# Optimization experiments

Measured on AMD Instinct MI355X. Metric: run time of the kernel, lower is better.

The kernel has to match this reference:

```python
import jax, jax.numpy as jnp
import numpy as np


def setup_inputs() -> dict:
    key = jax.random.key(0)
    k1, k2, k3, k4, k5 = jax.random.split(key, 5)
    B, F, S = 4096, 2048, 2048
    return {
        "weights": jax.random.normal(k1, (F + S, 3 * S), dtype=jnp.float32),
        "bias": jax.random.normal(k2, (3 * S,), dtype=jnp.float32),
        "input": jax.random.normal(k3, (B, F), dtype=jnp.float32),
        "old_h": jax.random.normal(k4, (B, S), dtype=jnp.float32),
        "old_c": jax.random.normal(k5, (B, S), dtype=jnp.float32),
    }


def reference(weights, bias, input, old_h, old_c):
    # LLTM cell (PyTorch C++ extension tutorial math):
    # X = [old_h, input]; gates = X @ W + b, split into 3 chunks of state_size.
    S = old_h.shape[1]
    X = jnp.concatenate([old_h, input], axis=1)            # (B, S+F)
    gate_weights = X @ weights + bias                       # (B, 3S)
    input_gate = jax.nn.sigmoid(gate_weights[:, :S])
    output_gate = jax.nn.sigmoid(gate_weights[:, S:2 * S])
    candidate_cell = jax.nn.elu(gate_weights[:, 2 * S:])
    new_cell = old_c + candidate_cell * input_gate          # (B, S)
    new_h = jnp.tanh(new_cell) * output_gate
    return new_h, new_cell
```

## Files before the change

### kernel.cpp

```cpp
#include <hip/hip_runtime.h>

typedef unsigned short u16;
typedef unsigned int u32;
typedef __attribute__((ext_vector_type(8))) __bf16 bf16x8;
typedef __attribute__((ext_vector_type(4))) float f32x4;
typedef __attribute__((ext_vector_type(4))) u32 u32x4;

#define MDIM 4096
#define KDIM 4096
#define NDIM 6144
#define SDIM 2048
#define KC   (KDIM / 32)

__device__ __forceinline__ u32 asu(float f) { return __float_as_uint(f); }

__device__ __forceinline__ void gld16(const void* g, void* l) {
    __builtin_amdgcn_global_load_lds(
        (const __attribute__((address_space(1))) u32*)g,
        (__attribute__((address_space(3))) u32*)l, 16, 0, 0);
}

__device__ __forceinline__ u32 pk(float a, float b) {
    return (asu(a) >> 16) | (asu(b) & 0xffff0000u);
}

__global__ __launch_bounds__(256) void prep(const float* __restrict__ W,
                                            const float* __restrict__ oldh,
                                            const float* __restrict__ inp,
                                            u32* __restrict__ Whl,
                                            u32* __restrict__ Ahl) {
    const int t = threadIdx.x;
    if (blockIdx.x < 6144) {
        __shared__ u32 wh[64][33];
        __shared__ u32 wl[64][33];
        const int n0 = (blockIdx.x % 96) * 64;
        const int k0 = (blockIdx.x / 96) * 64;
#pragma unroll
        for (int r = 0; r < 4; ++r) {
            int bid = t + r * 256;
            int nb = bid & 31;
            int kb = bid >> 5;
            const float* p0 = W + (size_t)(k0 + 2 * kb) * NDIM + n0 + 2 * nb;
            float2 w0 = *(const float2*)p0;
            float2 w1 = *(const float2*)(p0 + NDIM);
            float h00 = __uint_as_float(asu(w0.x) & 0xffff0000u);
            float h01 = __uint_as_float(asu(w0.y) & 0xffff0000u);
            float h10 = __uint_as_float(asu(w1.x) & 0xffff0000u);
            float h11 = __uint_as_float(asu(w1.y) & 0xffff0000u);
            wh[2 * nb][kb]     = pk(w0.x, w1.x);
            wh[2 * nb + 1][kb] = pk(w0.y, w1.y);
            wl[2 * nb][kb]     = pk(w0.x - h00, w1.x - h10);
            wl[2 * nb + 1][kb] = pk(w0.y - h01, w1.y - h11);
        }
        __syncthreads();
#pragma unroll
        for (int r = 0; r < 2; ++r) {
            int v = t + r * 256;
            int nl = v >> 3;
            int kw = (v & 7) * 4;
            int c  = (k0 >> 5) + (kw >> 4);
            int ww = kw & 15;
            size_t o = ((size_t)(n0 + nl) * KC + c) * 32 + ww;
            *(uint4*)(Whl + o)      = make_uint4(wh[nl][kw], wh[nl][kw + 1],
                                                 wh[nl][kw + 2], wh[nl][kw + 3]);
            *(uint4*)(Whl + o + 16) = make_uint4(wl[nl][kw], wl[nl][kw + 1],
                                                 wl[nl][kw + 2], wl[nl][kw + 3]);
        }
    } else {
        const int m = blockIdx.x - 6144;
#pragma unroll
        for (int rr = 0; rr < 2; ++rr) {
            int gk = t + rr * 256;
            int k = gk * 8;
            const float* src = (k < SDIM)
                                   ? (oldh + (size_t)m * SDIM + k)
                                   : (inp + (size_t)m * SDIM + (k - SDIM));
            float4 f0 = *(const float4*)src;
            float4 f1 = *(const float4*)(src + 4);
            int c = gk >> 2, g = gk & 3;
            size_t o = ((size_t)m * KC + c) * 32 + g * 4;
            *(uint4*)(Ahl + o) = make_uint4(pk(f0.x, f0.y), pk(f0.z, f0.w),
                                            pk(f1.x, f1.y), pk(f1.z, f1.w));
            float4 l0, l1;
            l0.x = f0.x - __uint_as_float(asu(f0.x) & 0xffff0000u);
            l0.y = f0.y - __uint_as_float(asu(f0.y) & 0xffff0000u);
            l0.z = f0.z - __uint_as_float(asu(f0.z) & 0xffff0000u);
            l0.w = f0.w - __uint_as_float(asu(f0.w) & 0xffff0000u);
            l1.x = f1.x - __uint_as_float(asu(f1.x) & 0xffff0000u);
            l1.y = f1.y - __uint_as_float(asu(f1.y) & 0xffff0000u);
            l1.z = f1.z - __uint_as_float(asu(f1.z) & 0xffff0000u);
            l1.w = f1.w - __uint_as_float(asu(f1.w) & 0xffff0000u);
            *(uint4*)(Ahl + o + 16) = make_uint4(pk(l0.x, l0.y), pk(l0.z, l0.w),
                                                 pk(l1.x, l1.y), pk(l1.z, l1.w));
        }
    }
}

__global__ __launch_bounds__(256, 2) void gemm_lltm(const u32* __restrict__ Whl,
                                                    const u32* __restrict__ Ahl,
                                                    const float* __restrict__ bias,
                                                    const float* __restrict__ oldc,
                                                    float* __restrict__ out) {
    __shared__ u16 As[2][128 * 64];
    __shared__ u16 Bs[2][192 * 64];
    const int t = threadIdx.x;
    const int lane = t & 63;
    const int wv = t >> 6;
    const int wm = wv >> 1;
    const int wn = wv & 1;
    const int row0 = blockIdx.y * 128;
    const int col0 = blockIdx.x * 64;

    f32x4 acc[3][4][2];
#pragma unroll
    for (int g = 0; g < 3; ++g)
#pragma unroll
        for (int i = 0; i < 4; ++i)
#pragma unroll
            for (int j = 0; j < 2; ++j)
                acc[g][i][j] = (f32x4){0.f, 0.f, 0.f, 0.f};

    const int sr8 = lane >> 3;
    const int lg  = (lane & 7) ^ sr8;

    const u32* aSrc[4];
#pragma unroll
    for (int i = 0; i < 4; ++i) {
        int r = wv * 32 + i * 8 + sr8;
        aSrc[i] = Ahl + (size_t)(row0 + r) * (KC * 32) + lg * 4;
    }
    const u32* bSrc[6];
#pragma unroll
    for (int p = 0; p < 6; ++p) {
        int r = wv * 48 + p * 8 + sr8;
        int n = (r >> 6) * SDIM + col0 + (r & 63);
        bSrc[p] = Whl + (size_t)n * (KC * 32) + lg * 4;
    }

    const int lm = lane & 15;
    const int q  = lane >> 4;
    const int sw = lm & 7;
    const int slotHi = q ^ sw;

    {
#pragma unroll
        for (int i = 0; i < 4; ++i)
            gld16(aSrc[i], &As[0][(wv * 32 + i * 8) * 64]);
#pragma unroll
        for (int p = 0; p < 6; ++p)
            gld16(bSrc[p], &Bs[0][(wv * 48 + p * 8) * 64]);
    }
    asm volatile("s_waitcnt vmcnt(0)" ::: "memory");
    __syncthreads();

    for (int c = 0; c < KC; ++c) {
        const int buf = c & 1;
        if (c + 1 < KC) {
#pragma unroll
            for (int i = 0; i < 4; ++i)
                gld16(aSrc[i] + (size_t)(c + 1) * 32,
                      &As[buf ^ 1][(wv * 32 + i * 8) * 64]);
#pragma unroll
            for (int p = 0; p < 6; ++p)
                gld16(bSrc[p] + (size_t)(c + 1) * 32,
                      &Bs[buf ^ 1][(wv * 48 + p * 8) * 64]);
        }

        bf16x8 ah[4], al[4];
#pragma unroll
        for (int i = 0; i < 4; ++i) {
            int mr = wm * 64 + i * 16 + lm;
            const u16* ap = &As[buf][mr * 64];
            ah[i] = *(const bf16x8*)(ap + slotHi * 8);
            al[i] = *(const bf16x8*)(ap + (slotHi ^ 4) * 8);
        }
        bf16x8 bh, bl;
        {
            const u16* bp = &Bs[buf][(wn * 32 + lm) * 64];
            bh = *(const bf16x8*)(bp + slotHi * 8);
            bl = *(const bf16x8*)(bp + (slotHi ^ 4) * 8);
        }

#pragma unroll
        for (int pc = 0; pc < 6; ++pc) {
            const int g = pc >> 1, j = pc & 1;
            bf16x8 cbh = bh, cbl = bl;
            if (pc < 5) {
                const int g2 = (pc + 1) >> 1, j2 = (pc + 1) & 1;
                const u16* bp =
                    &Bs[buf][(g2 * 64 + wn * 32 + j2 * 16 + lm) * 64];
                bh = *(const bf16x8*)(bp + slotHi * 8);
                bl = *(const bf16x8*)(bp + (slotHi ^ 4) * 8);
            }
            __builtin_amdgcn_s_setprio(1);
#pragma unroll
            for (int i = 0; i < 4; ++i)
                acc[g][i][j] = __builtin_amdgcn_mfma_f32_16x16x32_bf16(
                    ah[i], cbh, acc[g][i][j], 0, 0, 0);
#pragma unroll
            for (int i = 0; i < 4; ++i)
                acc[g][i][j] = __builtin_amdgcn_mfma_f32_16x16x32_bf16(
                    al[i], cbh, acc[g][i][j], 0, 0, 0);
#pragma unroll
            for (int i = 0; i < 4; ++i)
                acc[g][i][j] = __builtin_amdgcn_mfma_f32_16x16x32_bf16(
                    ah[i], cbl, acc[g][i][j], 0, 0, 0);
            __builtin_amdgcn_s_setprio(0);
        }
        asm volatile("s_waitcnt vmcnt(0)" ::: "memory");
        __syncthreads();
    }

    const int rq = q * 4;
#pragma unroll
    for (int j = 0; j < 2; ++j) {
        int scol = col0 + wn * 32 + j * 16 + lm;
        float b0v = bias[scol];
        float b1v = bias[SDIM + scol];
        float b2v = bias[2 * SDIM + scol];
#pragma unroll
        for (int i = 0; i < 4; ++i) {
#pragma unroll
            for (int r = 0; r < 4; ++r) {
                int row = row0 + wm * 64 + i * 16 + rq + r;
                float x0 = acc[0][i][j][r] + b0v;
                float x1 = acc[1][i][j][r] + b1v;
                float x2 = acc[2][i][j][r] + b2v;
                float ig = 1.f / (1.f + __expf(-x0));
                float og = 1.f / (1.f + __expf(-x1));
                float el = x2 > 0.f ? x2 : (__expf(x2) - 1.f);
                float nc = oldc[(size_t)row * SDIM + scol] + el * ig;
                float nh = tanhf(nc) * og;
                out[(size_t)row * SDIM + scol] = nh;
                out[(size_t)MDIM * SDIM + (size_t)row * SDIM + scol] = nc;
            }
        }
    }
}

extern "C" void kernel_launch(void* const* d_in, const int* in_sizes, int n_in,
                              void* d_out, int out_size, void* d_ws, size_t ws_size,
                              hipStream_t stream) {
    const float* W    = (const float*)d_in[0];
    const float* bias = (const float*)d_in[1];
    const float* inp  = (const float*)d_in[2];
    const float* oldh = (const float*)d_in[3];
    const float* oldc = (const float*)d_in[4];

    u32* Whl = (u32*)d_ws;
    u32* Ahl = Whl + (size_t)NDIM * KC * 32;

    prep<<<6144 + MDIM, 256, 0, stream>>>(W, oldh, inp, Whl, Ahl);
    gemm_lltm<<<dim3(SDIM / 64, MDIM / 128), 256, 0, stream>>>(Whl, Ahl, bias,
                                                               oldc,
                                                               (float*)d_out);
}
```

Before: 714.9 us.

## Load A fragments directly from global into registers, bypassing LDS

The A tile is no longer staged through shared memory. Each lane now loads its MFMA A fragments (hi and lo bf16 parts) straight from global memory into registers, double-buffered across an unrolled pair of iterations. This removes the LDS traffic and the shared-memory footprint for A, which may help occupancy. In exchange, each A row is loaded redundantly by both wn waves, global accesses are less coalesced, and register pressure rises.

```diff
diff --git a/kernel.cpp b/kernel.cpp
--- a/kernel.cpp
+++ b/kernel.cpp
@@ -101,7 +101,6 @@
                                                     const float* __restrict__ bias,
                                                     const float* __restrict__ oldc,
                                                     float* __restrict__ out) {
-    __shared__ u16 As[2][128 * 64];
     __shared__ u16 Bs[2][192 * 64];
     const int t = threadIdx.x;
     const int lane = t & 63;
@@ -123,12 +122,11 @@
     const int sr8 = lane >> 3;
     const int lg  = (lane & 7) ^ sr8;
 
-    const u32* aSrc[4];
-#pragma unroll
-    for (int i = 0; i < 4; ++i) {
-        int r = wv * 32 + i * 8 + sr8;
-        aSrc[i] = Ahl + (size_t)(row0 + r) * (KC * 32) + lg * 4;
-    }
+    const int lm = lane & 15;
+    const int q  = lane >> 4;
+    const int sw = lm & 7;
+    const int slotHi = q ^ sw;
+
     const u32* bSrc[6];
 #pragma unroll
     for (int p = 0; p < 6; ++p) {
@@ -137,42 +135,40 @@
         bSrc[p] = Whl + (size_t)n * (KC * 32) + lg * 4;
     }
 
-    const int lm = lane & 15;
-    const int q  = lane >> 4;
-    const int sw = lm & 7;
-    const int slotHi = q ^ sw;
+    const u32* aPtr[4];
+#pragma unroll
+    for (int i = 0; i < 4; ++i)
+        aPtr[i] = Ahl + (size_t)(row0 + wm * 64 + i * 16 + lm) * (KC * 32)
+                  + q * 4;
+
+    bf16x8 a0h[4], a0l[4], a1h[4], a1l[4];
 
     {
-#pragma unroll
-        for (int i = 0; i < 4; ++i)
-            gld16(aSrc[i], &As[0][(wv * 32 + i * 8) * 64]);
 #pragma unroll
         for (int p = 0; p < 6; ++p)
             gld16(bSrc[p], &Bs[0][(wv * 48 + p * 8) * 64]);
+#pragma unroll
+        for (int i = 0; i < 4; ++i) {
+            a0h[i] = __builtin_bit_cast(bf16x8, *(const u32x4*)(aPtr[i]));
+            a0l[i] = __builtin_bit_cast(bf16x8, *(const u32x4*)(aPtr[i] + 16));
+        }
     }
     asm volatile("s_waitcnt vmcnt(0)" ::: "memory");
     __syncthreads();
 
-    for (int c = 0; c < KC; ++c) {
-        const int buf = c & 1;
+    auto iter = [&](int c, int buf, bf16x8(&aH)[4], bf16x8(&aL)[4],
+                    bf16x8(&nH)[4], bf16x8(&nL)[4]) {
         if (c + 1 < KC) {
-#pragma unroll
-            for (int i = 0; i < 4; ++i)
-                gld16(aSrc[i] + (size_t)(c + 1) * 32,
-                      &As[buf ^ 1][(wv * 32 + i * 8) * 64]);
 #pragma unroll
             for (int p = 0; p < 6; ++p)
                 gld16(bSrc[p] + (size_t)(c + 1) * 32,
                       &Bs[buf ^ 1][(wv * 48 + p * 8) * 64]);
-        }
-
-        bf16x8 ah[4], al[4];
-#pragma unroll
-        for (int i = 0; i < 4; ++i) {
-            int mr = wm * 64 + i * 16 + lm;
-            const u16* ap = &As[buf][mr * 64];
-            ah[i] = *(const bf16x8*)(ap + slotHi * 8);
-            al[i] = *(const bf16x8*)(ap + (slotHi ^ 4) * 8);
+#pragma unroll
+            for (int i = 0; i < 4; ++i) {
+                const u32* ap = aPtr[i] + (size_t)(c + 1) * 32;
+                nH[i] = __builtin_bit_cast(bf16x8, *(const u32x4*)(ap));
+                nL[i] = __builtin_bit_cast(bf16x8, *(const u32x4*)(ap + 16));
+            }
         }
         bf16x8 bh, bl;
         {
@@ -180,7 +176,6 @@
             bh = *(const bf16x8*)(bp + slotHi * 8);
             bl = *(const bf16x8*)(bp + (slotHi ^ 4) * 8);
         }
-
 #pragma unroll
         for (int pc = 0; pc < 6; ++pc) {
             const int g = pc >> 1, j = pc & 1;
@@ -196,19 +191,24 @@
 #pragma unroll
             for (int i = 0; i < 4; ++i)
                 acc[g][i][j] = __builtin_amdgcn_mfma_f32_16x16x32_bf16(
-                    ah[i], cbh, acc[g][i][j], 0, 0, 0);
+                    aH[i], cbh, acc[g][i][j], 0, 0, 0);
 #pragma unroll
             for (int i = 0; i < 4; ++i)
                 acc[g][i][j] = __builtin_amdgcn_mfma_f32_16x16x32_bf16(
-                    al[i], cbh, acc[g][i][j], 0, 0, 0);
+                    aL[i], cbh, acc[g][i][j], 0, 0, 0);
 #pragma unroll
             for (int i = 0; i < 4; ++i)
                 acc[g][i][j] = __builtin_amdgcn_mfma_f32_16x16x32_bf16(
-                    ah[i], cbl, acc[g][i][j], 0, 0, 0);
+                    aH[i], cbl, acc[g][i][j], 0, 0, 0);
             __builtin_amdgcn_s_setprio(0);
         }
         asm volatile("s_waitcnt vmcnt(0)" ::: "memory");
         __syncthreads();
+    };
+
+    for (int cc = 0; cc < KC; cc += 2) {
+        iter(cc,     0, a0h, a0l, a1h, a1l);
+        iter(cc + 1, 1, a1h, a1l, a0h, a0l);
     }
 
     const int rq = q * 4;
```

Measured after the change: 841.1 us. 17.7% more time.
